# Optimization experiments

Measured on AMD Instinct MI355X. Metric: run time of the kernel, lower is better.

The kernel has to match this reference:

```python
import jax, jax.numpy as jnp
import numpy as np

NUM_HEADS = 16
HEAD_DIM = 64
MAX_POS = 2048  # max_position_embeddings


def setup_inputs() -> dict:
    key = jax.random.key(0)
    ks = jax.random.split(key, 8)
    B, S, H = 4, 1024, 1024
    s = 1.0 / np.sqrt(H)
    return {
        "hidden_states": jax.random.normal(ks[0], (B, S, H), jnp.float32),
        "attention_mask": jnp.zeros((B, 1, 1, S), jnp.float32),
        "Wq": jax.random.normal(ks[1], (H, H), jnp.float32) * s,
        "bq": jnp.zeros((H,), jnp.float32),
        "Wk": jax.random.normal(ks[2], (H, H), jnp.float32) * s,
        "bk": jnp.zeros((H,), jnp.float32),
        "Wv": jax.random.normal(ks[3], (H, H), jnp.float32) * s,
        "bv": jnp.zeros((H,), jnp.float32),
        "dist_emb": jax.random.normal(ks[4], (2 * MAX_POS - 1, HEAD_DIM), jnp.float32) * 0.02,
    }


def _split_heads(x):
    B, S, _ = x.shape
    return x.reshape(B, S, NUM_HEADS, HEAD_DIM).transpose(0, 2, 1, 3)  # [B,H,S,dh]


def reference(hidden_states, attention_mask, Wq, bq, Wk, bk, Wv, bv, dist_emb):
    B, S, _ = hidden_states.shape
    q = _split_heads(hidden_states @ Wq + bq)
    k = _split_heads(hidden_states @ Wk + bk)
    v = _split_heads(hidden_states @ Wv + bv)

    scores = jnp.einsum("bhld,bhrd->bhlr", q, k)

    # relative_key_query positional bias
    pos = jnp.arange(S)
    distance = pos[:, None] - pos[None, :]                 # [S,S]
    pe = dist_emb[distance + MAX_POS - 1]                   # [S,S,dh]
    scores = scores + jnp.einsum("bhld,lrd->bhlr", q, pe)
    scores = scores + jnp.einsum("bhrd,lrd->bhlr", k, pe)

    scores = scores / np.sqrt(HEAD_DIM).astype(np.float32)
    scores = scores + attention_mask                        # additive mask broadcast
    probs = jax.nn.softmax(scores, axis=-1)                 # dropout is identity in eval

    ctx = jnp.einsum("bhlr,bhrd->bhld", probs, v)
    ctx = ctx.transpose(0, 2, 1, 3).reshape(B, S, NUM_HEADS * HEAD_DIM)
    return ctx
```

## Files before the change

kernel.cpp:

```cpp
#include <hip/hip_runtime.h>
#include <hip/hip_bf16.h>

typedef __hip_bfloat16 bf16;
typedef __attribute__((ext_vector_type(8))) short bf16x8;
typedef __attribute__((ext_vector_type(4))) float f32x4;
typedef __attribute__((ext_vector_type(2))) unsigned int u32x2;

#define MFMA(a, b, c) __builtin_amdgcn_mfma_f32_16x16x32_bf16((a), (b), (c), 0, 0, 0)

static __device__ __forceinline__ float bf2f(bf16 b) { return __bfloat162float(b); }

static __device__ __forceinline__ unsigned pk2(float a, float b) {
    return __builtin_amdgcn_perm(__builtin_bit_cast(unsigned, b),
                                 __builtin_bit_cast(unsigned, a), 0x07060302u);
}

static __device__ __forceinline__ void gload16(const void* g, void* l) {
    __builtin_amdgcn_global_load_lds(
        (const __attribute__((address_space(1))) void*)g,
        (__attribute__((address_space(3))) void*)l, 16, 0, 0);
}

static __device__ __forceinline__ float quad_max(float x) {
    x = fmaxf(x, __shfl_xor(x, 16));
    x = fmaxf(x, __shfl_xor(x, 32));
    return x;
}
static __device__ __forceinline__ float quad_sum(float x) {
    x += __shfl_xor(x, 16);
    x += __shfl_xor(x, 32);
    return x;
}

__global__ void prep_convert(const float* __restrict__ X, const float* __restrict__ DE,
                             bf16* __restrict__ Xb, bf16* __restrict__ DEb) {
    int i = blockIdx.x * blockDim.x + threadIdx.x;
    if (i < 1048576) {
        float4 v = reinterpret_cast<const float4*>(X)[i];
        bf16* d = Xb + 4 * i;
        d[0] = __float2bfloat16(v.x); d[1] = __float2bfloat16(v.y);
        d[2] = __float2bfloat16(v.z); d[3] = __float2bfloat16(v.w);
    } else {
        int j = i - 1048576;
        if (j < 65520) {
            float4 v = reinterpret_cast<const float4*>(DE)[j];
            bf16* d = DEb + 4 * j;
            d[0] = __float2bfloat16(v.x); d[1] = __float2bfloat16(v.y);
            d[2] = __float2bfloat16(v.z); d[3] = __float2bfloat16(v.w);
        }
    }
}

__global__ void prep_transpose_w(const float* __restrict__ Wq, const float* __restrict__ Wk,
                                 const float* __restrict__ Wv, bf16* __restrict__ WTb) {
    const float* W = (blockIdx.z == 0) ? Wq : (blockIdx.z == 1) ? Wk : Wv;
    bf16* WT = WTb + (size_t)blockIdx.z * (1024u * 1024u);
    __shared__ float t[64][65];
    int tid = threadIdx.x;
    int col = tid & 63;
    int r4 = tid >> 6;
    int i0 = blockIdx.x * 64, o0 = blockIdx.y * 64;
    for (int it = 0; it < 16; ++it) {
        int row = it * 4 + r4;
        t[row][col] = W[(size_t)(i0 + row) * 1024 + o0 + col];
    }
    __syncthreads();
    for (int it = 0; it < 16; ++it) {
        int row = it * 4 + r4;
        WT[(size_t)(o0 + row) * 1024 + i0 + col] = __float2bfloat16(t[col][row]);
    }
}

__global__ __launch_bounds__(256, 2) void proj_gemm(
    const bf16* __restrict__ Xb, const bf16* __restrict__ WTb,
    const float* __restrict__ bq, const float* __restrict__ bk, const float* __restrict__ bv,
    bf16* __restrict__ Qb, bf16* __restrict__ Kb, bf16* __restrict__ VTb) {
    int proj = blockIdx.z;
    const bf16* W = WTb + (size_t)proj * (1024u * 1024u);
    const float* bias = (proj == 0) ? bq : (proj == 1) ? bk : bv;

    __shared__ bf16 XT[128][72];
    __shared__ bf16 WTt[128][72];

    int tid = threadIdx.x;
    int w = tid >> 6, lane = tid & 63, g = lane >> 4, li = lane & 15;
    int wr = w >> 1, wc = w & 1;
    int m0 = blockIdx.x * 128, n0 = blockIdx.y * 128;

    f32x4 acc[4][4];
    for (int mt = 0; mt < 4; mt++)
        for (int nt = 0; nt < 4; nt++) acc[mt][nt] = {0.f, 0.f, 0.f, 0.f};

    for (int ks = 0; ks < 16; ++ks) {
        for (int it = 0; it < 4; ++it) {
            int idx = tid + 256 * it;
            int row = idx >> 3, c = (idx & 7) * 8;
            *reinterpret_cast<bf16x8*>(&XT[row][c]) =
                *reinterpret_cast<const bf16x8*>(Xb + (size_t)(m0 + row) * 1024 + ks * 64 + c);
            *reinterpret_cast<bf16x8*>(&WTt[row][c]) =
                *reinterpret_cast<const bf16x8*>(W + (size_t)(n0 + row) * 1024 + ks * 64 + c);
        }
        __syncthreads();
        for (int kk = 0; kk < 2; ++kk) {
            bf16x8 af[4], bfr[4];
            for (int mt = 0; mt < 4; mt++)
                af[mt] = *reinterpret_cast<const bf16x8*>(&XT[64 * wr + 16 * mt + li][32 * kk + 8 * g]);
            for (int nt = 0; nt < 4; nt++)
                bfr[nt] = *reinterpret_cast<const bf16x8*>(&WTt[64 * wc + 16 * nt + li][32 * kk + 8 * g]);
            for (int mt = 0; mt < 4; mt++)
                for (int nt = 0; nt < 4; nt++)
                    acc[mt][nt] = MFMA(af[mt], bfr[nt], acc[mt][nt]);
        }
        __syncthreads();
    }

    for (int mt = 0; mt < 4; mt++)
        for (int nt = 0; nt < 4; nt++) {
            int n = n0 + 64 * wc + 16 * nt + li;
            int h = n >> 6, d = n & 63;
            float bv_ = bias[n];
            for (int r = 0; r < 4; r++) {
                int m = m0 + 64 * wr + 16 * mt + 4 * g + r;
                int b = m >> 10, s = m & 1023;
                bf16 o = __float2bfloat16(acc[mt][nt][r] + bv_);
                if (proj == 0)      Qb[((size_t)(b * 16 + h) * 1024 + s) * 64 + d] = o;
                else if (proj == 1) Kb[((size_t)(b * 16 + h) * 1024 + s) * 64 + d] = o;
                else                VTb[((size_t)(b * 16 + h) * 64 + d) * 1024 + s] = o;
            }
        }
}

__global__ __launch_bounds__(512, 4) void attn_fused(
    const bf16* __restrict__ Qg, const bf16* __restrict__ Kg,
    const bf16* __restrict__ VTg, const bf16* __restrict__ DEb,
    const float* __restrict__ mask, float* __restrict__ out) {
    const int S = 1024, D = 64;
    const float C8 = 0.18033688011112042f;
    int p_ = blockIdx.x;
    int idx = p_ >> 3;
    int bh = (p_ & 7) * 8 + (idx >> 3);
    int qb = idx & 7;
    int b = bh >> 4, h = bh & 15;
    int L0 = qb * 128;

    int tid = threadIdx.x;
    int w = tid >> 6, lane = tid & 63, g = lane >> 4, li = lane & 15;

    __shared__ __align__(16) char smem[81664];
    bf16 (*Mb)[64] = reinterpret_cast<bf16(*)[64]>(smem + 81408);

    const char* Kh = (const char*)(Kg + (size_t)bh * S * D);
    const char* Vh = (const char*)(VTg + (size_t)bh * D * S);
    const char* DEc = (const char*)DEb;
    const float* maskb = mask + (size_t)b * S;

    int sw = (li & 7) << 4;
    int c0 = (16 * g) ^ sw;
    int c1 = (64 + 16 * g) ^ sw;
    const char* KbL = smem + li * 128;
    int gsel = (w < 4) ? (3 - w) : (7 - w);
    const char* KaL = smem + (16 * gsel + li) * 128;
    const char* Vb_ = smem + 8192 + li * 128;
    const char* Db_ = smem + 16384;

    int srow = tid >> 3;
    int sc = 16 * ((lane & 7) ^ (lane >> 3));

    bf16x8 qa0, qa1;
    {
        const bf16* qrow = Qg + (size_t)bh * S * D + (size_t)(L0 + 16 * w + li) * D;
        qa0 = *reinterpret_cast<const bf16x8*>(qrow + 8 * g);
        qa1 = *reinterpret_cast<const bf16x8*>(qrow + 32 + 8 * g);
    }

    const char* qdb = smem + 40960 + 2688 * w + 170 * li - 8 * g;
    const char* kdb = smem + 62464 + 1176 * g + 32 * w + 2 * li + 30;
    char* qsp = smem + 40960 + 2688 * w + 168 * li + 8 * g;
    char* ksp = smem + 62464 + 296 * (16 * gsel + li) + ((w < 4) ? 0 : 128) + 8 * g;
    char* Pp  = smem + 40960 + 2688 * w + 144 * li;

    int de00 = L0 + 1984;
    int jb = de00 % 192;
    {
        gload16(Kh + (size_t)srow * 128 + sc, smem + w * 1024);
        gload16(Vh + (size_t)srow * 2048 + sc, smem + 8192 + w * 1024);
        #pragma unroll
        for (int c = 0; c < 3; ++c) {
            int pb = jb + 64 * c; if (pb >= 192) pb -= 192;
            gload16(DEc + (size_t)(de00 + 64 * c + srow) * 128 + sc,
                    smem + 16384 + pb * 128 + w * 1024);
        }
        if (tid < 64) Mb[0][tid] = __float2bfloat16(maskb[tid]);
    }

    f32x4 acc_o[4];
    for (int dt = 0; dt < 4; dt++) acc_o[dt] = {0.f, 0.f, 0.f, 0.f};
    float m_run = -1e30f, l_run = 0.f;

    __syncthreads();

    for (int kt = 0; kt < 16; ++kt) {
        int r0 = kt * 64;
        bool has_next = (kt < 15);
        int jbw = jb + 16 * w;

        if (kt) {
            gload16(Vh + (size_t)srow * 2048 + (size_t)r0 * 2 + sc, smem + 8192 + w * 1024);
        }

        __builtin_amdgcn_s_setprio(1);
        f32x4 s_acc[4];
        #pragma unroll
        for (int nt = 0; nt < 4; ++nt) {
            bf16x8 kb0 = *reinterpret_cast<const bf16x8*>(KbL + nt * 2048 + c0);
            bf16x8 kb1 = *reinterpret_cast<const bf16x8*>(KbL + nt * 2048 + c1);
            f32x4 z = {0.f, 0.f, 0.f, 0.f};
            z = MFMA(kb0, qa0, z);
            z = MFMA(kb1, qa1, z);
            s_acc[nt] = z;
        }
        {
            bf16x8 ka0 = *reinterpret_cast<const bf16x8*>(KaL + c0);
            bf16x8 ka1 = *reinterpret_cast<const bf16x8*>(KaL + c1);
            #pragma unroll
            for (int jt = 0; jt < 5; ++jt) {
                int x = jbw + 16 * jt + li;
                if (x >= 192) x -= 192;
                const char* dp = Db_ + x * 128;
                bf16x8 d0 = *reinterpret_cast<const bf16x8*>(dp + c0);
                bf16x8 d1 = *reinterpret_cast<const bf16x8*>(dp + c1);
                f32x4 aq = {0.f, 0.f, 0.f, 0.f};
                aq = MFMA(d0, qa0, aq);
                aq = MFMA(d1, qa1, aq);
                f32x4 ak = {0.f, 0.f, 0.f, 0.f};
                ak = MFMA(d0, ka0, ak);
                ak = MFMA(d1, ka1, ak);
                u32x2 uq = {pk2(aq[0], aq[1]), pk2(aq[2], aq[3])};
                *reinterpret_cast<u32x2*>(qsp + 32 * jt) = uq;
                u32x2 uk = {pk2(ak[0], ak[1]), pk2(ak[2], ak[3])};
                *reinterpret_cast<u32x2*>(ksp + 32 * jt) = uk;
            }
        }
        __builtin_amdgcn_s_setprio(0);
        __syncthreads();

        float sM;
        if (has_next) {
            int r0n = r0 + 64;
            int dlo = de00 - 64 * (kt + 1);
            int jbN = (jb >= 64) ? jb - 64 : jb + 128;
            gload16(Kh + (size_t)(r0n + srow) * 128 + sc, smem + w * 1024);
            gload16(DEc + (size_t)(dlo + srow) * 128 + sc,
                    smem + 16384 + jbN * 128 + w * 1024);
            if (tid < 64) sM = maskb[r0n + tid];
            jb = jbN;
        }

        float u[4][4];
        float lmax = -1e30f;
        #pragma unroll
        for (int nt = 0; nt < 4; ++nt) {
            unsigned long long mraw =
                *reinterpret_cast<const unsigned long long*>(&Mb[kt & 1][16 * nt + 4 * g]);
            #pragma unroll
            for (int r = 0; r < 4; ++r) {
                float qd = bf2f(*reinterpret_cast<const bf16*>(qdb + (126 - 32 * nt - 2 * r)));
                float kd = bf2f(*reinterpret_cast<const bf16*>(kdb + (4736 * nt + 294 * r)));
                float mk = __builtin_bit_cast(float,
                    (unsigned)((mraw >> (16 * r)) & 0xffffull) << 16);
                float uu = s_acc[nt][r] + qd + kd;
                uu = __builtin_fmaf(mk, 8.0f, uu);
                u[nt][r] = uu;
                lmax = fmaxf(lmax, uu);
            }
        }
        float tm = quad_max(lmax);
        bool noskip = !__all(tm <= m_run);
        float scl = 1.0f;
        if (noskip) {
            float mnew = fmaxf(m_run, tm);
            scl = exp2f((m_run - mnew) * C8);
            m_run = mnew;
        }
        float nmc = -m_run * C8;
        float pv[4][4];
        #pragma unroll
        for (int nt = 0; nt < 4; ++nt)
            #pragma unroll
            for (int r = 0; r < 4; ++r)
                pv[nt][r] = exp2f(__builtin_fmaf(u[nt][r], C8, nmc));
        float t0 = (pv[0][0] + pv[0][1]) + (pv[0][2] + pv[0][3]);
        float t1 = (pv[1][0] + pv[1][1]) + (pv[1][2] + pv[1][3]);
        float t2 = (pv[2][0] + pv[2][1]) + (pv[2][2] + pv[2][3]);
        float t3 = (pv[3][0] + pv[3][1]) + (pv[3][2] + pv[3][3]);
        float qs = quad_sum((t0 + t1) + (t2 + t3));
        if (noskip) {
            l_run = l_run * scl + qs;
            #pragma unroll
            for (int dt = 0; dt < 4; dt++) acc_o[dt] *= scl;
        } else {
            l_run += qs;
        }

        #pragma unroll
        for (int nt = 0; nt < 4; ++nt) {
            u32x2 pp = {pk2(pv[nt][0], pv[nt][1]), pk2(pv[nt][2], pv[nt][3])};
            *reinterpret_cast<u32x2*>(Pp + 32 * nt + 8 * g) = pp;
        }
        bf16x8 pb0 = *reinterpret_cast<const bf16x8*>(Pp + 16 * g);
        bf16x8 pb1 = *reinterpret_cast<const bf16x8*>(Pp + 64 + 16 * g);

        __builtin_amdgcn_s_setprio(1);
        #pragma unroll
        for (int dt = 0; dt < 4; dt++) {
            bf16x8 va0 = *reinterpret_cast<const bf16x8*>(Vb_ + dt * 2048 + c0);
            bf16x8 va1 = *reinterpret_cast<const bf16x8*>(Vb_ + dt * 2048 + c1);
            acc_o[dt] = MFMA(va0, pb0, acc_o[dt]);
            acc_o[dt] = MFMA(va1, pb1, acc_o[dt]);
        }
        __builtin_amdgcn_s_setprio(0);

        if (has_next && tid < 64) Mb[(kt + 1) & 1][tid] = __float2bfloat16(sM);
        __syncthreads();
    }

    float inv = 1.0f / l_run;
    float (*OT)[68] = reinterpret_cast<float (*)[68]>(smem);
    #pragma unroll
    for (int dt = 0; dt < 4; dt++)
        #pragma unroll
        for (int r = 0; r < 4; r++)
            OT[16 * w + li][16 * dt + 4 * g + r] = acc_o[dt][r] * inv;
    __syncthreads();
    {
        int q = tid >> 2, seg = tid & 3;
        float* gout = out + ((size_t)(b * 1024 + L0 + q)) * 1024 + h * 64 + 16 * seg;
        #pragma unroll
        for (int j = 0; j < 4; ++j)
            *reinterpret_cast<float4*>(gout + 4 * j) =
                *reinterpret_cast<const float4*>(&OT[q][16 * seg + 4 * j]);
    }
}

extern "C" void kernel_launch(void* const* d_in, const int* in_sizes, int n_in,
                              void* d_out, int out_size, void* d_ws, size_t ws_size,
                              hipStream_t stream) {
    const float* X   = (const float*)d_in[0];
    const float* msk = (const float*)d_in[1];
    const float* Wq  = (const float*)d_in[2];
    const float* bq  = (const float*)d_in[3];
    const float* Wk  = (const float*)d_in[4];
    const float* bk  = (const float*)d_in[5];
    const float* Wv  = (const float*)d_in[6];
    const float* bv  = (const float*)d_in[7];
    const float* DE  = (const float*)d_in[8];
    float* out = (float*)d_out;

    bf16* ws  = (bf16*)d_ws;
    bf16* Xb  = ws;
    bf16* WTb = ws + 4194304;
    bf16* DEb = ws + 7340032;
    bf16* Qb  = ws + 7602176;
    bf16* Kb  = ws + 11796480;
    bf16* VTb = ws + 15990784;

    prep_convert<<<4352, 256, 0, stream>>>(X, DE, Xb, DEb);
    prep_transpose_w<<<dim3(16, 16, 3), 256, 0, stream>>>(Wq, Wk, Wv, WTb);
    proj_gemm<<<dim3(32, 8, 3), 256, 0, stream>>>(Xb, WTb, bq, bk, bv, Qb, Kb, VTb);
    attn_fused<<<512, 512, 0, stream>>>(Qb, Kb, VTb, DEb, msk, out);
}
```

Measured before the change: 141.5 us.

## Use direct global-to-LDS loads with XOR-swizzled tiles and XCD-aware block remap in projection GEMM

The projection GEMM now stages its X and W tiles with global_load_lds 16-byte transfers straight into a single shared buffer. The tiles use an XOR swizzle on 16-byte chunks instead of padded rows, which targets LDS bank conflicts on the MFMA fragment reads. Block indices are flattened and remapped so consecutive blocks on each XCD share projection and tile neighbourhoods for better L2 reuse, and launch bounds rise to allow three blocks per CU. The main loop stays single-buffered with two barriers per step, so load latency is still mostly exposed, and the swizzle and async-load indexing must stay consistent.

```diff
diff --git a/kernel.cpp b/kernel.cpp
--- a/kernel.cpp
+++ b/kernel.cpp
@@ -71,47 +71,73 @@
     }
 }
 
-__global__ __launch_bounds__(256, 2) void proj_gemm(
+__global__ __launch_bounds__(256, 3) void proj_gemm(
     const bf16* __restrict__ Xb, const bf16* __restrict__ WTb,
     const float* __restrict__ bq, const float* __restrict__ bk, const float* __restrict__ bv,
     bf16* __restrict__ Qb, bf16* __restrict__ Kb, bf16* __restrict__ VTb) {
-    int proj = blockIdx.z;
+    int id = blockIdx.x;
+    int swz = (id & 7) * 96 + (id >> 3);
+    int proj = swz >> 8;
+    int rem = swz & 255;
+    int m0 = (rem & 31) * 128;
+    int n0 = (rem >> 5) * 128;
+
     const bf16* W = WTb + (size_t)proj * (1024u * 1024u);
     const float* bias = (proj == 0) ? bq : (proj == 1) ? bk : bv;
 
-    __shared__ bf16 XT[128][72];
-    __shared__ bf16 WTt[128][72];
+    __shared__ __align__(16) char ps[32768];
 
     int tid = threadIdx.x;
     int w = tid >> 6, lane = tid & 63, g = lane >> 4, li = lane & 15;
     int wr = w >> 1, wc = w & 1;
-    int m0 = blockIdx.x * 128, n0 = blockIdx.y * 128;
+
+    int srow8 = lane >> 3;
+    int ssc = 16 * ((lane & 7) ^ srow8);
+
+    int sw = (li & 7) << 4;
+    const char* xb = ps + (size_t)(64 * wr + li) * 128;
+    const char* wb = ps + 16384 + (size_t)(64 * wc + li) * 128;
 
     f32x4 acc[4][4];
     for (int mt = 0; mt < 4; mt++)
         for (int nt = 0; nt < 4; nt++) acc[mt][nt] = {0.f, 0.f, 0.f, 0.f};
 
+    #pragma unroll
+    for (int c = 0; c < 4; ++c) {
+        int rb = 32 * c + 8 * w;
+        gload16((const char*)Xb + (size_t)(m0 + rb + srow8) * 2048 + ssc, ps + rb * 128);
+        gload16((const char*)W + (size_t)(n0 + rb + srow8) * 2048 + ssc, ps + 16384 + rb * 128);
+    }
+
     for (int ks = 0; ks < 16; ++ks) {
-        for (int it = 0; it < 4; ++it) {
-            int idx = tid + 256 * it;
-            int row = idx >> 3, c = (idx & 7) * 8;
-            *reinterpret_cast<bf16x8*>(&XT[row][c]) =
-                *reinterpret_cast<const bf16x8*>(Xb + (size_t)(m0 + row) * 1024 + ks * 64 + c);
-            *reinterpret_cast<bf16x8*>(&WTt[row][c]) =
-                *reinterpret_cast<const bf16x8*>(W + (size_t)(n0 + row) * 1024 + ks * 64 + c);
-        }
         __syncthreads();
+        #pragma unroll
         for (int kk = 0; kk < 2; ++kk) {
+            int cc = (64 * kk + 16 * g) ^ sw;
             bf16x8 af[4], bfr[4];
+            #pragma unroll
             for (int mt = 0; mt < 4; mt++)
-                af[mt] = *reinterpret_cast<const bf16x8*>(&XT[64 * wr + 16 * mt + li][32 * kk + 8 * g]);
+                af[mt] = *reinterpret_cast<const bf16x8*>(xb + mt * 2048 + cc);
+            #pragma unroll
             for (int nt = 0; nt < 4; nt++)
-                bfr[nt] = *reinterpret_cast<const bf16x8*>(&WTt[64 * wc + 16 * nt + li][32 * kk + 8 * g]);
+                bfr[nt] = *reinterpret_cast<const bf16x8*>(wb + nt * 2048 + cc);
+            #pragma unroll
             for (int mt = 0; mt < 4; mt++)
+                #pragma unroll
                 for (int nt = 0; nt < 4; nt++)
                     acc[mt][nt] = MFMA(af[mt], bfr[nt], acc[mt][nt]);
         }
-        __syncthreads();
+        if (ks < 15) {
+            __syncthreads();
+            #pragma unroll
+            for (int c = 0; c < 4; ++c) {
+                int rb = 32 * c + 8 * w;
+                gload16((const char*)Xb + (size_t)(m0 + rb + srow8) * 2048 + (ks + 1) * 128 + ssc,
+                        ps + rb * 128);
+                gload16((const char*)W + (size_t)(n0 + rb + srow8) * 2048 + (ks + 1) * 128 + ssc,
+                        ps + 16384 + rb * 128);
+            }
+        }
     }
 
     for (int mt = 0; mt < 4; mt++)
@@ -366,6 +392,6 @@
 
     prep_convert<<<4352, 256, 0, stream>>>(X, DE, Xb, DEb);
     prep_transpose_w<<<dim3(16, 16, 3), 256, 0, stream>>>(Wq, Wk, Wv, WTb);
-    proj_gemm<<<dim3(32, 8, 3), 256, 0, stream>>>(Xb, WTb, bq, bk, bv, Qb, Kb, VTb);
+    proj_gemm<<<768, 256, 0, stream>>>(Xb, WTb, bq, bk, bv, Qb, Kb, VTb);
     attn_fused<<<512, 512, 0, stream>>>(Qb, Kb, VTb, DEb, msk, out);
 }
```

Measured after the change: 154.3 us. 1.09x slower.
